# Optimization experiments

Hardware: AMD Instinct MI355X
Metric: run time of the kernel (lower is better)

The kernel has to match this reference:

```python
import jax, jax.numpy as jnp
import numpy as np

B, L, H, V = 256, 2048, 64, 64


def setup_inputs() -> dict:
    key = jax.random.key(0)
    ks = jax.random.split(key, 16)
    s = 0.05
    return {
        "seq": jax.random.randint(ks[0], (B, L), 0, V),
        "embed": jax.random.normal(ks[1], (V, H), jnp.float32) * s,
        "W1": jax.random.normal(ks[2], (2 * H, H), jnp.float32) * s,
        "b1": jnp.zeros((2 * H,), jnp.float32),
        "W2": jax.random.normal(ks[3], (H, 2 * H), jnp.float32) * s,
        "b2": jnp.zeros((H,), jnp.float32),
        "gamma": jnp.ones((H,), jnp.float32),
        "beta": jnp.zeros((H,), jnp.float32),
        "Wk": jax.random.normal(ks[4], (H, H), jnp.float32) * s,
        "Wv": jax.random.normal(ks[5], (H, H), jnp.float32) * s,
        "Wq": jax.random.normal(ks[6], (H, H), jnp.float32) * s,
        "Wrp": jax.random.normal(ks[7], (H, H), jnp.float32) * s,
        "brp": jnp.zeros((H,), jnp.float32),
        "Wout": jax.random.normal(ks[8], (V, H), jnp.float32) * s,
        "bout": jnp.zeros((V,), jnp.float32),
    }


def reference(seq, embed, W1, b1, W2, b2, gamma, beta, Wk, Wv, Wq, Wrp, brp, Wout, bout):
    # encode: LayerNorm(e + FF(e))
    e = embed[seq]                                   # [B, L, H]
    ff = jnp.maximum(e @ W1.T + b1, 0.0) @ W2.T + b2  # [B, L, H]
    h = e + ff
    mu = h.mean(-1, keepdims=True)
    var = ((h - mu) ** 2).mean(-1, keepdims=True)    # torch LN: biased var, eps=1e-5
    hs = (h - mu) / jnp.sqrt(var + 1e-5) * gamma + beta

    # precompute k/v for the first L-1 steps (batched GEMM)
    k_all = hs[:, :-1] @ Wk.T                         # [B, L-1, H]
    v_all = hs[:, :-1] @ Wv.T                         # [B, L-1, H]
    # F.normalize(k, dim=-1): k / max(||k||, 1e-12)
    k_n = k_all / jnp.maximum(jnp.linalg.norm(k_all, axis=-1, keepdims=True), 1e-12)

    def step(M, kv):
        k, v = kv                                      # each [B, H]
        vp = jnp.einsum('bij,bj->bi', M, k)
        M = M + jnp.einsum('bi,bj->bij', v - vp, k)    # rank-1 delta update
        return M, None

    M0 = jnp.zeros((B, H, H), hs.dtype)
    M, _ = jax.lax.scan(step, M0, (jnp.swapaxes(k_n, 0, 1), jnp.swapaxes(v_all, 0, 1)))

    q = hs[:, -1] @ Wq.T                               # [B, H]
    r = jnp.einsum('bij,bj->bi', M, q) @ Wrp.T + brp
    return r @ Wout.T + bout                           # [B, V]
```

## Files before the change

kernel.cpp:

```cpp
#include <hip/hip_runtime.h>


#define DPP_ADD_F32(x, ctrl, rm, bm, bc)                                      \
  (x) = (x) + __int_as_float(__builtin_amdgcn_update_dpp(                     \
            0, __float_as_int(x), (ctrl), (rm), (bm), (bc)))

__device__ __forceinline__ float wave_sum64(float x) {
  DPP_ADD_F32(x, 0x111, 0xf, 0xf, true);
  DPP_ADD_F32(x, 0x112, 0xf, 0xf, true);
  DPP_ADD_F32(x, 0x114, 0xf, 0xf, true);
  DPP_ADD_F32(x, 0x118, 0xf, 0xf, true);
  DPP_ADD_F32(x, 0x142, 0xa, 0xf, false);
  DPP_ADD_F32(x, 0x143, 0xc, 0xf, false);
  return __int_as_float(__builtin_amdgcn_readlane(__float_as_int(x), 63));
}

__device__ __forceinline__ float readlane_f(float x, int lane) {
  return __int_as_float(__builtin_amdgcn_readlane(__float_as_int(x), lane));
}

__global__ __launch_bounds__(64) void build_tables(
    const float* __restrict__ embed, const float* __restrict__ W1,
    const float* __restrict__ b1, const float* __restrict__ W2,
    const float* __restrict__ b2, const float* __restrict__ gamma,
    const float* __restrict__ beta, const float* __restrict__ Wk,
    const float* __restrict__ Wv, const float* __restrict__ Wq,
    float* __restrict__ k_tab, float* __restrict__ v_tab,
    float* __restrict__ q_tab) {
  __shared__ float Wbuf[8448];
  __shared__ float e_s[64];
  __shared__ float f1_s[128];
  __shared__ float hs_s[64];
  const int tok = blockIdx.x;
  const int l = threadIdx.x;

  const float e = embed[tok * 64 + l];
  e_s[l] = e;
  for (int i = 0; i < 128; ++i) Wbuf[i * 65 + l] = W1[i * 64 + l];
  __syncthreads();

  float a0 = b1[l], a1 = b1[l + 64];
#pragma unroll
  for (int h = 0; h < 64; ++h) {
    a0 = fmaf(e_s[h], Wbuf[l * 65 + h], a0);
    a1 = fmaf(e_s[h], Wbuf[(l + 64) * 65 + h], a1);
  }
  f1_s[l] = fmaxf(a0, 0.f);
  f1_s[l + 64] = fmaxf(a1, 0.f);
  __syncthreads();

  for (int i = 0; i < 128; ++i)
    Wbuf[(i >> 1) * 131 + (i & 1) * 64 + l] = W2[i * 64 + l];
  __syncthreads();

  float acc = b2[l];
#pragma unroll
  for (int j = 0; j < 128; ++j) acc = fmaf(f1_s[j], Wbuf[l * 131 + j], acc);
  const float hval = e + acc;

  const float mu = wave_sum64(hval) * (1.f / 64.f);
  const float d = hval - mu;
  const float var = wave_sum64(d * d) * (1.f / 64.f);
  const float hs = d * (1.f / sqrtf(var + 1e-5f)) * gamma[l] + beta[l];
  hs_s[l] = hs;
  __syncthreads();

  for (int i = 0; i < 64; ++i) {
    Wbuf[i * 65 + l] = Wk[i * 64 + l];
    Wbuf[4224 + i * 65 + l] = Wv[i * 64 + l];
  }
  __syncthreads();
  float kk = 0.f, vv = 0.f;
#pragma unroll
  for (int h = 0; h < 64; ++h) {
    kk = fmaf(hs_s[h], Wbuf[l * 65 + h], kk);
    vv = fmaf(hs_s[h], Wbuf[4224 + l * 65 + h], vv);
  }
  __syncthreads();
  for (int i = 0; i < 64; ++i) Wbuf[i * 65 + l] = Wq[i * 64 + l];
  __syncthreads();
  float qq = 0.f;
#pragma unroll
  for (int h = 0; h < 64; ++h) qq = fmaf(hs_s[h], Wbuf[l * 65 + h], qq);

  float nrm = fmaxf(sqrtf(wave_sum64(kk * kk)), 1e-12f);
  k_tab[tok * 64 + l] = kk / nrm;
  v_tab[tok * 64 + l] = vv;
  q_tab[tok * 64 + l] = qq;
}

__global__ __launch_bounds__(64) void build_gram(
    const float* __restrict__ k_tab, const float* __restrict__ q_tab,
    const float* __restrict__ v_tab, float2* __restrict__ GV,
    float* __restrict__ KQ) {
  __shared__ float k_s[4160];
  __shared__ float q_s[64];
  const int a = blockIdx.x;
  const int l = threadIdx.x;
  for (int i = 0; i < 64; ++i) k_s[i * 65 + l] = k_tab[i * 64 + l];
  q_s[l] = q_tab[a * 64 + l];
  __syncthreads();
  float g = 0.f, kq = 0.f;
#pragma unroll
  for (int h = 0; h < 64; ++h) {
    g = fmaf(k_s[a * 65 + h], k_s[l * 65 + h], g);
    kq = fmaf(q_s[h], k_s[l * 65 + h], kq);
  }
  GV[a * 64 + l] = make_float2(-g, v_tab[a * 64 + l]);
  KQ[a * 64 + l] = kq;
}

__global__ __launch_bounds__(64, 1) void scan_head(
    const int* __restrict__ seq, const float2* __restrict__ GVg,
    const float* __restrict__ KQ, const float* __restrict__ Wrp,
    const float* __restrict__ brp, const float* __restrict__ Wout,
    const float* __restrict__ bout, float* __restrict__ out) {
  __shared__ float2 GV_s[4160];
  __shared__ float tmp[64];
  const int b = blockIdx.x;
  const int l = threadIdx.x;

#pragma unroll
  for (int i = 0; i < 32; ++i)
    ((float4*)GV_s)[l + 64 * i] = ((const float4*)GVg)[l + 64 * i];
  GV_s[4096 + l] = make_float2(0.f, 0.f);
  __syncthreads();

  const int* tokp = seq + b * 2048;
  const int qt = tokp[2047];
  float y = KQ[qt * 64 + l];
  float r = 0.f;

  int tokA = (l == 0) ? 64 : tokp[2047 - l];
  int tokB = tokp[2047 - 64 - l];

  float2 colX[8], colY[8];
  int selX[8], selY[8];

#pragma unroll
  for (int k = 0; k < 8; ++k) {
    selX[k] = __builtin_amdgcn_readlane(tokA, k);
    colX[k] = GV_s[selX[k] * 64 + l];
  }
  float s_prev = 0.f;
  float cf_cur = 0.f;
  float p_cur = readlane_f(y, selX[0] & 63);

  auto BATCH = [&](float2 (&cC)[8], int (&sC)[8], float2 (&cN)[8],
                   int (&sN)[8], int tokvec, int lane_base) {
#pragma unroll
    for (int k = 0; k < 8; ++k) {
      sN[k] = __builtin_amdgcn_readlane(tokvec, lane_base + k);
      cN[k] = GV_s[sN[k] * 64 + l];
    }
#pragma unroll
    for (int k = 0; k < 8; ++k) {
      const int nsel = ((k < 7) ? sC[k + 1] : sN[0]) & 63;
      const float p_next = readlane_f(y, nsel);
      const float s_i = fmaf(cf_cur, s_prev, p_cur);
      const float cf_next = readlane_f(cC[k].x, nsel);
      y = fmaf(s_i, cC[k].x, y);
      r = fmaf(s_i, cC[k].y, r);
      p_cur = p_next;
      cf_cur = cf_next;
      s_prev = s_i;
    }
  };

  for (int blk = 0; blk < 32; ++blk) {
    BATCH(colX, selX, colY, selY, tokA, 8);
    BATCH(colY, selY, colX, selX, tokA, 16);
    BATCH(colX, selX, colY, selY, tokA, 24);
    BATCH(colY, selY, colX, selX, tokA, 32);
    BATCH(colX, selX, colY, selY, tokA, 40);
    BATCH(colY, selY, colX, selX, tokA, 48);
    BATCH(colX, selX, colY, selY, tokA, 56);
    BATCH(colY, selY, colX, selX, tokB, 0);
    tokA = tokB;
    tokB = (blk + 2 < 32) ? tokp[2047 - 64 * (blk + 2) - l] : 64;
  }

  float* Wb = (float*)GV_s;
  tmp[l] = r;
  __syncthreads();
  for (int i = 0; i < 64; ++i) {
    Wb[i * 65 + l] = Wrp[i * 64 + l];
    Wb[4160 + i * 65 + l] = Wout[i * 64 + l];
  }
  __syncthreads();
  float acc = brp[l];
#pragma unroll
  for (int j = 0; j < 64; ++j) acc = fmaf(tmp[j], Wb[l * 65 + j], acc);
  __syncthreads();
  tmp[l] = acc;
  __syncthreads();
  float o = bout[l];
#pragma unroll
  for (int i = 0; i < 64; ++i) o = fmaf(tmp[i], Wb[4160 + l * 65 + i], o);
  out[b * 64 + l] = o;
}

extern "C" void kernel_launch(void* const* d_in, const int* in_sizes, int n_in,
                              void* d_out, int out_size, void* d_ws,
                              size_t ws_size, hipStream_t stream) {
  const int* seq = (const int*)d_in[0];
  const float* embed = (const float*)d_in[1];
  const float* W1 = (const float*)d_in[2];
  const float* b1 = (const float*)d_in[3];
  const float* W2 = (const float*)d_in[4];
  const float* b2 = (const float*)d_in[5];
  const float* gamma = (const float*)d_in[6];
  const float* beta = (const float*)d_in[7];
  const float* Wk = (const float*)d_in[8];
  const float* Wv = (const float*)d_in[9];
  const float* Wq = (const float*)d_in[10];
  const float* Wrp = (const float*)d_in[11];
  const float* brp = (const float*)d_in[12];
  const float* Wout = (const float*)d_in[13];
  const float* bout = (const float*)d_in[14];

  float* wsf = (float*)d_ws;
  float* k_tab = wsf;
  float* v_tab = wsf + 4096;
  float* q_tab = wsf + 8192;
  float2* GV = (float2*)(wsf + 12288);
  float* KQ = wsf + 20480;

  build_tables<<<64, 64, 0, stream>>>(embed, W1, b1, W2, b2, gamma, beta, Wk,
                                      Wv, Wq, k_tab, v_tab, q_tab);
  build_gram<<<64, 64, 0, stream>>>(k_tab, q_tab, v_tab, GV, KQ);
  scan_head<<<256, 64, 0, stream>>>(seq, GV, KQ, Wrp, brp, Wout, bout,
                                    (float*)d_out);
}
```

Measured before the change: 148.7 us.

## Block the serial scan recurrence into groups of four with precomputed coupling

Restructures the per-step scalar recurrence in the scan kernel into blocks of four steps. The pairwise coupling coefficients within each block are precomputed one block ahead by readlane, and the four y values are read at once, so the serial dependency chain on y shrinks from one per step to one per four steps. Column loads are prefetched three groups ahead through a four-slot rotating buffer. In exchange it issues more readlane and FMA instructions per step and uses more registers, and the reassociated arithmetic can change rounding slightly.

```diff
diff --git a/kernel.cpp b/kernel.cpp
--- a/kernel.cpp
+++ b/kernel.cpp
@@ -134,48 +134,75 @@
   int tokA = (l == 0) ? 64 : tokp[2047 - l];
   int tokB = tokp[2047 - 64 - l];
 
-  float2 colX[8], colY[8];
-  int selX[8], selY[8];
-
-#pragma unroll
-  for (int k = 0; k < 8; ++k) {
-    selX[k] = __builtin_amdgcn_readlane(tokA, k);
-    colX[k] = GV_s[selX[k] * 64 + l];
-  }
-  float s_prev = 0.f;
-  float cf_cur = 0.f;
-  float p_cur = readlane_f(y, selX[0] & 63);
-
-  auto BATCH = [&](float2 (&cC)[8], int (&sC)[8], float2 (&cN)[8],
-                   int (&sN)[8], int tokvec, int lane_base) {
-#pragma unroll
-    for (int k = 0; k < 8; ++k) {
-      sN[k] = __builtin_amdgcn_readlane(tokvec, lane_base + k);
-      cN[k] = GV_s[sN[k] * 64 + l];
+  float2 colR[4][4];
+  int selS[4][4];
+  float cfb[2][6];
+
+#pragma unroll
+  for (int g = 0; g < 3; ++g) {
+#pragma unroll
+    for (int k = 0; k < 4; ++k) {
+      selS[g][k] = __builtin_amdgcn_readlane(tokA, 4 * g + k);
+      colR[g][k] = GV_s[selS[g][k] * 64 + l];
     }
-#pragma unroll
-    for (int k = 0; k < 8; ++k) {
-      const int nsel = ((k < 7) ? sC[k + 1] : sN[0]) & 63;
-      const float p_next = readlane_f(y, nsel);
-      const float s_i = fmaf(cf_cur, s_prev, p_cur);
-      const float cf_next = readlane_f(cC[k].x, nsel);
-      y = fmaf(s_i, cC[k].x, y);
-      r = fmaf(s_i, cC[k].y, r);
-      p_cur = p_next;
-      cf_cur = cf_next;
-      s_prev = s_i;
+  }
+  {
+    const int a1 = selS[0][1] & 63, a2 = selS[0][2] & 63, a3 = selS[0][3] & 63;
+    cfb[0][0] = readlane_f(colR[0][0].x, a1);
+    cfb[0][1] = readlane_f(colR[0][0].x, a2);
+    cfb[0][2] = readlane_f(colR[0][0].x, a3);
+    cfb[0][3] = readlane_f(colR[0][1].x, a2);
+    cfb[0][4] = readlane_f(colR[0][1].x, a3);
+    cfb[0][5] = readlane_f(colR[0][2].x, a3);
+  }
+
+  for (int blk = 0; blk < 32; ++blk) {
+#pragma unroll
+    for (int ss = 0; ss < 16; ++ss) {
+      const int c0 = ss & 3;
+      const int c1 = (ss + 1) & 3;
+      const int c3 = (ss + 3) & 3;
+      const int cur = ss & 1;
+      const int nxt = cur ^ 1;
+
+      const int lb = 4 * (ss + 3);
+#pragma unroll
+      for (int k = 0; k < 4; ++k) {
+        selS[c3][k] =
+            __builtin_amdgcn_readlane(lb < 64 ? tokA : tokB, (lb & 63) + k);
+        colR[c3][k] = GV_s[selS[c3][k] * 64 + l];
+      }
+
+      const int a1 = selS[c1][1] & 63, a2 = selS[c1][2] & 63,
+                a3 = selS[c1][3] & 63;
+      cfb[nxt][0] = readlane_f(colR[c1][0].x, a1);
+      cfb[nxt][1] = readlane_f(colR[c1][0].x, a2);
+      cfb[nxt][2] = readlane_f(colR[c1][0].x, a3);
+      cfb[nxt][3] = readlane_f(colR[c1][1].x, a2);
+      cfb[nxt][4] = readlane_f(colR[c1][1].x, a3);
+      cfb[nxt][5] = readlane_f(colR[c1][2].x, a3);
+
+      const float p0 = readlane_f(y, selS[c0][0] & 63);
+      const float p1 = readlane_f(y, selS[c0][1] & 63);
+      const float p2 = readlane_f(y, selS[c0][2] & 63);
+      const float p3 = readlane_f(y, selS[c0][3] & 63);
+
+      const float s0 = p0;
+      const float s1 = fmaf(cfb[cur][0], s0, p1);
+      const float s2 = fmaf(cfb[cur][3], s1, fmaf(cfb[cur][1], s0, p2));
+      const float s3 = fmaf(
+          cfb[cur][5], s2,
+          fmaf(cfb[cur][4], s1, fmaf(cfb[cur][2], s0, p3)));
+
+      y = fmaf(s0, colR[c0][0].x, y);
+      r = fmaf(s0, colR[c0][0].y, r);
+      y = fmaf(s1, colR[c0][1].x, y);
+      r = fmaf(s1, colR[c0][1].y, r);
+      y = fmaf(s2, colR[c0][2].x, y);
+      r = fmaf(s2, colR[c0][2].y, r);
+      y = fmaf(s3, colR[c0][3].x, y);
+      r = fmaf(s3, colR[c0][3].y, r);
     }
-  };
-
-  for (int blk = 0; blk < 32; ++blk) {
-    BATCH(colX, selX, colY, selY, tokA, 8);
-    BATCH(colY, selY, colX, selX, tokA, 16);
-    BATCH(colX, selX, colY, selY, tokA, 24);
-    BATCH(colY, selY, colX, selX, tokA, 32);
-    BATCH(colX, selX, colY, selY, tokA, 40);
-    BATCH(colY, selY, colX, selX, tokA, 48);
-    BATCH(colX, selX, colY, selY, tokA, 56);
-    BATCH(colY, selY, colX, selX, tokB, 0);
     tokA = tokB;
     tokB = (blk + 2 < 32) ? tokp[2047 - 64 * (blk + 2) - l] : 64;
   }
```

Measured after the change: 153.8 us. 3.4% more time.
